# Kernel tuning notes

Measured on AMD Instinct MI355X. Metric: run time of the kernel, lower is better.

## Reference

```python
import jax, jax.numpy as jnp
import numpy as np
from jax import lax

DIM, DIN, NST, DTR, K = 96, 192, 16, 6, 4
B, H, W = 2, 56, 56
MID, SEMID = 24, 24
EPS = 1e-5


def _ln(x, g, b):
    m = x.mean(-1, keepdims=True)
    v = ((x - m) ** 2).mean(-1, keepdims=True)
    return (x - m) / jnp.sqrt(v + EPS) * g + b


def _bn(x, g, b, m, v):  # eval-mode BatchNorm2d, NCHW
    return (x - m[None, :, None, None]) / jnp.sqrt(v[None, :, None, None] + EPS) * g[None, :, None, None] + b[None, :, None, None]


def _conv(x, w, pad, groups=1):
    return lax.conv_general_dilated(x, w, (1, 1), [(pad, pad), (pad, pad)],
                                    dimension_numbers=('NCHW', 'OIHW', 'NCHW'),
                                    feature_group_count=groups)


def _vssm(xn, in_proj_w, conv_w, conv_b, x_proj_w, dt_proj_w, dt_proj_b,
          A_log, Ds, out_norm_g, out_norm_b, out_proj_w):
    Bz, Hh, Ww, C = xn.shape
    L = Hh * Ww
    xz = xn @ in_proj_w.T                      # (B,H,W,2*Din)
    xc, z = jnp.split(xz, 2, axis=-1)
    xc = xc.transpose(0, 3, 1, 2)              # (B,Din,H,W)
    xc = _conv(xc, conv_w, pad=1, groups=DIN) + conv_b[None, :, None, None]
    xc = jax.nn.silu(xc)
    # 4 scan directions: row-major, col-major, and their reverses
    x1 = xc.reshape(Bz, DIN, L)
    x2 = xc.transpose(0, 1, 3, 2).reshape(Bz, DIN, L)
    xs = jnp.stack([x1, x2], axis=1)
    xs = jnp.concatenate([xs, jnp.flip(xs, axis=-1)], axis=1)   # (B,4,Din,L)
    x_dbl = jnp.einsum('bkdl,kcd->bkcl', xs, x_proj_w)          # (B,4,dtR+2N,L)
    dts, Bs, Cs = jnp.split(x_dbl, [DTR, DTR + NST], axis=2)
    delta = jax.nn.softplus(jnp.einsum('bkrl,kdr->bkdl', dts, dt_proj_w)
                            + dt_proj_b[None, :, :, None])      # (B,4,Din,L)
    A = -jnp.exp(A_log).reshape(K, DIN, NST)
    dA = jnp.exp(jnp.einsum('bkdl,kdn->bkdln', delta, A))       # (B,4,Din,L,N)
    dBu = jnp.einsum('bkdl,bknl,bkdl->bkdln', delta, Bs, xs)

    def comb(c1, c2):
        a1, b1 = c1
        a2, b2 = c2
        return (a1 * a2, a2 * b1 + b2)

    _, hs = lax.associative_scan(comb, (dA, dBu), axis=3)       # h_t = dA_t h_{t-1} + dBu_t
    ys = jnp.einsum('bkdln,bknl->bkdl', hs, Cs) + Ds.reshape(1, K, DIN, 1) * xs
    inv = jnp.flip(ys[:, 2:4], axis=-1)

    def t_back(y):
        return y.reshape(Bz, DIN, Ww, Hh).transpose(0, 1, 3, 2).reshape(Bz, DIN, L)

    y = ys[:, 0] + t_back(ys[:, 1]) + inv[:, 0] + t_back(inv[:, 1])
    y = y.reshape(Bz, DIN, Hh, Ww).transpose(0, 2, 3, 1)        # (B,H,W,Din)
    y = _ln(y, out_norm_g, out_norm_b) * jax.nn.silu(z)
    return y @ out_proj_w.T                                      # (B,H,W,dim)


def setup_inputs() -> dict:
    key = jax.random.key(0)
    ks = jax.random.split(key, 16)
    r = lambda k, s, sc=0.05: (jax.random.normal(k, s, dtype=jnp.float32) * sc)
    d = {}
    d['x'] = jax.random.normal(ks[0], (B, DIM, H, W), dtype=jnp.float32)
    d['norm1_g'] = jnp.ones((DIM,), jnp.float32); d['norm1_b'] = jnp.zeros((DIM,), jnp.float32)
    d['in_proj_w'] = r(ks[1], (2 * DIN, DIM))
    d['conv_w'] = r(ks[2], (DIN, 1, 3, 3), 0.2); d['conv_b'] = jnp.zeros((DIN,), jnp.float32)
    d['x_proj_w'] = r(ks[3], (K, DTR + 2 * NST, DIN))
    d['dt_proj_w'] = r(ks[4], (K, DIN, DTR), 0.2)
    d['dt_proj_b'] = jnp.full((K, DIN), -2.0, jnp.float32)
    d['A_log'] = jnp.log(jnp.broadcast_to(jnp.arange(1, NST + 1, dtype=jnp.float32), (K * DIN, NST)) + 0.0)
    d['Ds'] = jnp.ones((K * DIN,), jnp.float32)
    d['out_norm_g'] = jnp.ones((DIN,), jnp.float32); d['out_norm_b'] = jnp.zeros((DIN,), jnp.float32)
    d['out_proj_w'] = r(ks[5], (DIM, DIN))
    d['scale1'] = jnp.full((DIM,), 0.1, jnp.float32)
    d['norm2_g'] = jnp.ones((DIM,), jnp.float32); d['norm2_b'] = jnp.zeros((DIM,), jnp.float32)
    d['lc_w1'] = r(ks[6], (MID, DIM, 1, 1), 0.1)
    d['lc_g1'] = jnp.ones((MID,), jnp.float32); d['lc_b1'] = jnp.zeros((MID,), jnp.float32)
    d['lc_m1'] = jnp.zeros((MID,), jnp.float32); d['lc_v1'] = jnp.ones((MID,), jnp.float32)
    d['lc_w2'] = r(ks[7], (MID, MID, 3, 3), 0.1)
    d['lc_g2'] = jnp.ones((MID,), jnp.float32); d['lc_b2'] = jnp.zeros((MID,), jnp.float32)
    d['lc_m2'] = jnp.zeros((MID,), jnp.float32); d['lc_v2'] = jnp.ones((MID,), jnp.float32)
    d['lc_w3'] = r(ks[8], (DIM, MID, 1, 1), 0.1)
    d['lc_g3'] = jnp.ones((DIM,), jnp.float32); d['lc_b3'] = jnp.zeros((DIM,), jnp.float32)
    d['lc_m3'] = jnp.zeros((DIM,), jnp.float32); d['lc_v3'] = jnp.ones((DIM,), jnp.float32)
    d['se_w1'] = r(ks[9], (SEMID, DIM), 0.1)
    d['se_w2'] = r(ks[10], (DIM, SEMID), 0.1)
    d['scale2'] = jnp.full((DIM,), 0.1, jnp.float32)
    return d


def reference(x, norm1_g, norm1_b, in_proj_w, conv_w, conv_b, x_proj_w, dt_proj_w,
              dt_proj_b, A_log, Ds, out_norm_g, out_norm_b, out_proj_w, scale1,
              norm2_g, norm2_b, lc_w1, lc_g1, lc_b1, lc_m1, lc_v1, lc_w2, lc_g2,
              lc_b2, lc_m2, lc_v2, lc_w3, lc_g3, lc_b3, lc_m3, lc_v3, se_w1,
              se_w2, scale2):
    x_hwc = x.transpose(0, 2, 3, 1)                    # (B,H,W,C)
    vl = _vssm(_ln(x_hwc, norm1_g, norm1_b), in_proj_w, conv_w, conv_b,
               x_proj_w, dt_proj_w, dt_proj_b, A_log, Ds,
               out_norm_g, out_norm_b, out_proj_w)
    vl = vl + scale1 * x_hwc                           # scaled residual
    vb = _ln(vl, norm2_g, norm2_b).transpose(0, 3, 1, 2)  # (B,C,H,W)
    h = jax.nn.relu(_bn(_conv(vb, lc_w1, pad=0), lc_g1, lc_b1, lc_m1, lc_v1))
    h = jax.nn.relu(_bn(_conv(h, lc_w2, pad=1), lc_g2, lc_b2, lc_m2, lc_v2))
    h = _bn(_conv(h, lc_w3, pad=0), lc_g3, lc_b3, lc_m3, lc_v3)
    # SE channel attention
    w = h.mean(axis=(2, 3))                            # (B,C)
    w = jax.nn.sigmoid(jax.nn.relu(w @ se_w1.T) @ se_w2.T)
    h = h * w[:, :, None, None]
    return h + scale2[None, :, None, None] * vl.transpose(0, 3, 1, 2)
```

## Files before the change

### kernel.cpp

```cpp
#include <hip/hip_runtime.h>
#include <math.h>

#define DIMC 96
#define DINC 192
#define NSTC 16
#define DTRC 6
#define KDIR 4
#define BB   2
#define HH   56
#define WWD  56
#define LL   3136
#define NPIX (BB*LL)
#define EPSF 1e-5f
#define NCH  56
#define LC   56
#define NCHAIN (BB*KDIR*DINC)
#define NCOLS 152

#define OFF_HENDT  0u
#define OFF_SUMDT  1376256u
#define OFF_XCRAW  602112u
#define OFF_ZS     1806336u
#define OFF_XCONV  3010560u
#define OFF_DTS    4214784u
#define OFF_BCB    4365312u
#define OFF_BCC    4766720u
#define OFF_XSCANT 5168128u
#define OFF_CUMD   9985024u
#define OFF_YS     14801920u
#define OFF_YT     9985024u
#define OFF_VL     11189248u
#define OFF_H1     11791360u
#define OFF_H2     11941888u
#define OFF_POOL   12092416u
#define OFF_SEW    12092608u
#define OFF_H3     0u

__device__ __forceinline__ float siluf(float x) { return x / (1.f + __expf(-x)); }
__device__ __forceinline__ float softplusf(float x) {
    return fmaxf(x, 0.f) + __logf(1.f + __expf(-fabsf(x)));
}
__device__ __forceinline__ float fexp2(float x) {
#if __has_builtin(__builtin_amdgcn_exp2f)
    return __builtin_amdgcn_exp2f(x);
#else
    return exp2f(x);
#endif
}
#define LOG2E 1.44269504088896f

__global__ __launch_bounds__(256) void gemm1_k(const float* __restrict__ x,
                                               const float* __restrict__ g,
                                               const float* __restrict__ bt,
                                               const float* __restrict__ W,
                                               float* __restrict__ xcr,
                                               float* __restrict__ zs) {
    __shared__ float xT[64 * 97];
    __shared__ float wT[96 * 100];
    __shared__ float mA[64], iA[64];
    int row0 = blockIdx.x * 64;
    int b = row0 / LL, pos0 = row0 % LL;
    int c0 = blockIdx.y * 96;
    for (int f = threadIdx.x; f < 96 * 16; f += 256) {
        int ch = f >> 4, po = (f & 15) * 4;
        float4 v = *(const float4*)&x[((size_t)b * DIMC + ch) * LL + pos0 + po];
        xT[(po + 0) * 97 + ch] = v.x; xT[(po + 1) * 97 + ch] = v.y;
        xT[(po + 2) * 97 + ch] = v.z; xT[(po + 3) * 97 + ch] = v.w;
    }
    for (int f = threadIdx.x; f < 96 * 24; f += 256) {
        int r = f / 24, kq = (f % 24) * 4;
        *(float4*)&wT[r * 100 + kq] = *(const float4*)&W[(size_t)(c0 + r) * DIMC + kq];
    }
    __syncthreads();
    if (threadIdx.x < 64) {
        float s = 0.f, q = 0.f;
        const float* xr = &xT[threadIdx.x * 97];
        for (int c = 0; c < 96; ++c) { float v = xr[c]; s += v; q = fmaf(v, v, q); }
        float m = s * (1.f / 96.f);
        mA[threadIdx.x] = m;
        iA[threadIdx.x] = rsqrtf(q * (1.f / 96.f) - m * m + EPSF);
    }
    __syncthreads();
    for (int e = threadIdx.x; e < 64 * 96; e += 256) {
        int row = e / 96, col = e - row * 96;
        float v = xT[row * 97 + col];
        xT[row * 97 + col] = (v - mA[row]) * iA[row] * g[col] + bt[col];
    }
    __syncthreads();
    int tc = threadIdx.x & 15, tr = threadIdx.x >> 4;
    float acc[4][6] = {};
    for (int k = 0; k < 96; ++k) {
        float xv[4], wv[6];
#pragma unroll
        for (int i = 0; i < 4; ++i) xv[i] = xT[(4 * tr + i) * 97 + k];
#pragma unroll
        for (int j = 0; j < 6; ++j) wv[j] = wT[(tc + 16 * j) * 100 + k];
#pragma unroll
        for (int i = 0; i < 4; ++i)
#pragma unroll
            for (int j = 0; j < 6; ++j) acc[i][j] = fmaf(xv[i], wv[j], acc[i][j]);
    }
    int pos = pos0 + 4 * tr;
    if (c0 < DINC) {
#pragma unroll
        for (int j = 0; j < 6; ++j) {
            int col = c0 + tc + 16 * j;
            float4 v = make_float4(acc[0][j], acc[1][j], acc[2][j], acc[3][j]);
            *(float4*)&xcr[((size_t)b * DINC + col) * LL + pos] = v;
        }
    } else {
#pragma unroll
        for (int i = 0; i < 4; ++i)
#pragma unroll
            for (int j = 0; j < 6; ++j) {
                int zc = c0 - DINC + tc + 16 * j;
                zs[(size_t)(row0 + 4 * tr + i) * DINC + zc] = siluf(acc[i][j]);
            }
    }
}

__global__ __launch_bounds__(448) void dwconv_k(const float* __restrict__ xcr,
                                                const float* __restrict__ cw,
                                                const float* __restrict__ cb,
                                                float* __restrict__ xconv) {
    __shared__ float P[56 * 57];
    int bd = blockIdx.x;
    int d = bd % DINC;
    size_t base = (size_t)bd * LL;
    for (int t = threadIdx.x; t < LL; t += 448)
        P[(t / 56) * 57 + (t % 56)] = xcr[base + t];
    float wk[9];
#pragma unroll
    for (int q = 0; q < 9; ++q) wk[q] = cw[d * 9 + q];
    float bias = cb[d];
    __syncthreads();
    for (int t = threadIdx.x; t < LL; t += 448) {
        int h = t / 56, w = t % 56;
        float acc = bias;
#pragma unroll
        for (int ky = 0; ky < 3; ++ky) {
            int y = h + ky - 1;
            if ((unsigned)y >= 56u) continue;
#pragma unroll
            for (int kx = 0; kx < 3; ++kx) {
                int xq = w + kx - 1;
                if ((unsigned)xq >= 56u) continue;
                acc = fmaf(wk[ky * 3 + kx], P[y * 57 + xq], acc);
            }
        }
        xconv[base + t] = siluf(acc);
    }
}

__global__ __launch_bounds__(256) void gemmx_k(const float* __restrict__ xconv,
                                               const float* __restrict__ xpw,
                                               float* __restrict__ dts,
                                               float* __restrict__ bcB,
                                               float* __restrict__ bcC,
                                               float* __restrict__ xscanT) {
    __shared__ float xT[64 * 49];
    __shared__ float wT[NCOLS * 52];
    int row0 = blockIdx.x * 64;
    int b = row0 / LL, pos0 = row0 % LL;
    int tc = threadIdx.x & 15, tr = threadIdx.x >> 4;
    float acc[4][10] = {};
    for (int kc = 0; kc < 4; ++kc) {
        if (kc) __syncthreads();
        for (int f = threadIdx.x; f < 48 * 16; f += 256) {
            int dd = f >> 4, po = (f & 15) * 4;
            float4 v = *(const float4*)&xconv[((size_t)b * DINC + kc * 48 + dd) * LL + pos0 + po];
            xT[(po + 0) * 49 + dd] = v.x; xT[(po + 1) * 49 + dd] = v.y;
            xT[(po + 2) * 49 + dd] = v.z; xT[(po + 3) * 49 + dd] = v.w;
        }
        for (int f = threadIdx.x; f < NCOLS * 12; f += 256) {
            int r = f / 12, kq = (f % 12) * 4;
            *(float4*)&wT[r * 52 + kq] = *(const float4*)&xpw[(size_t)r * DINC + kc * 48 + kq];
        }
        __syncthreads();
        for (int k = 0; k < 48; ++k) {
            float xv[4], wv[10];
#pragma unroll
            for (int i = 0; i < 4; ++i) xv[i] = xT[(4 * tr + i) * 49 + k];
#pragma unroll
            for (int j = 0; j < 10; ++j) {
                int c = tc + 16 * j;
                wv[j] = (c < NCOLS) ? wT[c * 52 + k] : 0.f;
            }
#pragma unroll
            for (int i = 0; i < 4; ++i)
#pragma unroll
                for (int j = 0; j < 10; ++j) acc[i][j] = fmaf(xv[i], wv[j], acc[i][j]);
        }
        for (int f = threadIdx.x; f < 64 * 48; f += 256) {
            int i = f / 48, dd = f - 48 * (f / 48);
            float v = xT[i * 49 + dd];
            int pos = pos0 + i;
            int hh = pos / 56, w = pos - 56 * hh;
            int lt = w * 56 + hh;
            size_t bb = (size_t)b * KDIR;
            int col = kc * 48 + dd;
            xscanT[((bb + 0) * LL + pos) * DINC + col] = v;
            xscanT[((bb + 1) * LL + lt) * DINC + col] = v;
            xscanT[((bb + 2) * LL + (LL - 1 - pos)) * DINC + col] = v;
            xscanT[((bb + 3) * LL + (LL - 1 - lt)) * DINC + col] = v;
        }
    }
#pragma unroll
    for (int i = 0; i < 4; ++i) {
        int pos = pos0 + 4 * tr + i;
        int h = pos / 56, w = pos - 56 * h;
        int lt = w * 56 + h;
#pragma unroll
        for (int j = 0; j < 10; ++j) {
            int c = tc + 16 * j;
            if (c >= NCOLS) continue;
            int k = c / 38, idx = c - 38 * k;
            int l = (k == 0) ? pos : (k == 1) ? lt : (k == 2) ? (LL - 1 - pos) : (LL - 1 - lt);
            size_t rb = (size_t)(b * KDIR + k) * LL + l;
            float v = acc[i][j];
            if (idx < DTRC)    dts[rb * DTRC + idx] = v;
            else if (idx < 22) bcB[rb * NSTC + (idx - 6)] = v;
            else               bcC[rb * NSTC + (idx - 22)] = v;
        }
    }
}

__global__ __launch_bounds__(64) void pass1_k(const float* __restrict__ dts,
                                              const float* __restrict__ bcB,
                                              const float* __restrict__ bcC,
                                              const float* __restrict__ alog,
                                              const float* __restrict__ dtw,
                                              const float* __restrict__ dtb,
                                              const float* __restrict__ xscanT,
                                              float* __restrict__ hendT,
                                              float* __restrict__ sumdT,
                                              float* __restrict__ ysT,
                                              float* __restrict__ cumdT) {
    __shared__ float sdt[LC * 7];
    __shared__ float sB[LC * 16];
    __shared__ float sC[LC * 16];
    int blk = blockIdx.x;
    int c = blk % NCH;
    int dtile = (blk / NCH) % 3;
    int bk = blk / (NCH * 3);
    int k = bk & 3;
    int l0 = c * LC;
    int t = threadIdx.x;
    int d = dtile * 64 + t;
    const float* dsrc = dts + ((size_t)bk * LL + l0) * DTRC;
    for (int f = t; f < LC * DTRC; f += 64) sdt[(f / DTRC) * 7 + (f % DTRC)] = dsrc[f];
    const float* bB = bcB + ((size_t)bk * LL + l0) * NSTC;
    const float* bC = bcC + ((size_t)bk * LL + l0) * NSTC;
    for (int f = t; f < LC * NSTC; f += 64) { sB[f] = bB[f]; sC[f] = bC[f]; }
    float wr[DTRC];
    {
        const float* wp = dtw + ((size_t)k * DINC + d) * DTRC;
#pragma unroll
        for (int r = 0; r < DTRC; ++r) wr[r] = wp[r];
    }
    float bias = dtb[k * DINC + d];
    float An2[NSTC];
    {
        const float* ap = alog + ((size_t)(k * DINC + d)) * NSTC;
#pragma unroll
        for (int n = 0; n < NSTC; ++n) An2[n] = -__expf(ap[n]) * LOG2E;
    }
    __syncthreads();
    float h[NSTC];
#pragma unroll
    for (int n = 0; n < NSTC; ++n) h[n] = 0.f;
    float cum = 0.f;
    const float* xrow = xscanT + ((size_t)bk * LL + l0) * DINC + d;
    float* yrow = ysT + ((size_t)bk * LL + l0) * DINC + d;
    float* crow = cumdT + ((size_t)bk * LL + l0) * DINC + d;
#pragma unroll 8
    for (int s = 0; s < LC; ++s) {
        float acc = bias;
#pragma unroll
        for (int r = 0; r < DTRC; ++r) acc = fmaf(wr[r], sdt[s * 7 + r], acc);
        float dv = softplusf(acc);
        float xv = xrow[(size_t)s * DINC];
        cum += dv;
        float dx = dv * xv;
        const float4* B4 = (const float4*)&sB[s * 16];
        const float4* C4 = (const float4*)&sC[s * 16];
        float y = 0.f;
#pragma unroll
        for (int nq = 0; nq < 4; ++nq) {
            float4 Bv = B4[nq], Cv = C4[nq];
            float e0 = fexp2(An2[nq * 4 + 0] * dv);
            h[nq * 4 + 0] = fmaf(e0, h[nq * 4 + 0], dx * Bv.x);
            y = fmaf(h[nq * 4 + 0], Cv.x, y);
            float e1 = fexp2(An2[nq * 4 + 1] * dv);
            h[nq * 4 + 1] = fmaf(e1, h[nq * 4 + 1], dx * Bv.y);
            y = fmaf(h[nq * 4 + 1], Cv.y, y);
            float e2 = fexp2(An2[nq * 4 + 2] * dv);
            h[nq * 4 + 2] = fmaf(e2, h[nq * 4 + 2], dx * Bv.z);
            y = fmaf(h[nq * 4 + 2], Cv.z, y);
            float e3 = fexp2(An2[nq * 4 + 3] * dv);
            h[nq * 4 + 3] = fmaf(e3, h[nq * 4 + 3], dx * Bv.w);
            y = fmaf(h[nq * 4 + 3], Cv.w, y);
        }
        yrow[(size_t)s * DINC] = y;
        crow[(size_t)s * DINC] = cum;
    }
#pragma unroll
    for (int n = 0; n < NSTC; ++n)
        hendT[((size_t)(bk * NCH + c) * NSTC + n) * DINC + d] = h[n];
    sumdT[(size_t)(bk * NCH + c) * DINC + d] = cum;
}

__global__ __launch_bounds__(256) void scan2_k(float* __restrict__ hendT,
                                               const float* __restrict__ sumdT,
                                               const float* __restrict__ alog) {
    int gid = blockIdx.x * 256 + threadIdx.x;
    int d = gid % DINC;
    int n = (gid / DINC) % NSTC;
    int bk = gid / (DINC * NSTC);
    int k = bk & 3;
    float An2 = -__expf(alog[((size_t)(k * DINC + d)) * NSTC + n]) * LOG2E;
    float h = 0.f;
#pragma unroll 4
    for (int c = 0; c < NCH; ++c) {
        size_t idx = ((size_t)(bk * NCH + c) * NSTC + n) * DINC + d;
        float he = hendT[idx];
        float sd = sumdT[(size_t)(bk * NCH + c) * DINC + d];
        hendT[idx] = h;
        h = fmaf(fexp2(An2 * sd), h, he);
    }
}

__global__ __launch_bounds__(256) void pass2_k(const float* __restrict__ bcC,
                                               const float* __restrict__ alog,
                                               const float* __restrict__ hpreT,
                                               const float* __restrict__ cumdT,
                                               float* __restrict__ ysT) {
    __shared__ float sA2[DINC * 17];
    __shared__ float sH[DINC * 17];
    __shared__ float sC[LC * NSTC];
    int blk = blockIdx.x;
    int c = blk % NCH;
    int bk = blk / NCH;
    int k = bk & 3;
    int l0 = c * LC;
    int tid = threadIdx.x;
    const float* ap = alog + (size_t)k * DINC * NSTC;
    for (int f = tid; f < DINC * NSTC; f += 256) {
        int dq = f / NSTC, n = f % NSTC;
        sA2[dq * 17 + n] = -__expf(ap[f]) * LOG2E;
    }
    for (int f = tid; f < DINC * NSTC; f += 256) {
        int n = f / DINC, dq = f % DINC;
        sH[dq * 17 + n] = hpreT[((size_t)(bk * NCH + c) * NSTC + n) * DINC + dq];
    }
    const float* bC = bcC + ((size_t)bk * LL + l0) * NSTC;
    for (int f = tid; f < LC * NSTC; f += 256) sC[f] = bC[f];
    __syncthreads();
    for (int e = tid; e < LC * DINC; e += 256) {
        int li = e / DINC, d = e - DINC * (e / DINC);
        size_t gq = ((size_t)bk * LL + l0 + li) * DINC + d;
        float cd = cumdT[gq];
        float y = ysT[gq];
        const float* A = &sA2[d * 17];
        const float* Hp = &sH[d * 17];
        const float* Cp = &sC[li * NSTC];
#pragma unroll
        for (int n = 0; n < NSTC; ++n)
            y = fmaf(Hp[n] * fexp2(A[n] * cd), Cp[n], y);
        ysT[gq] = y;
    }
}

__global__ __launch_bounds__(256) void combine_k(const float* __restrict__ ysT,
                                                 const float* __restrict__ xscanT,
                                                 const float* __restrict__ dsv,
                                                 float* __restrict__ ytT) {
    __shared__ float sD[DINC];
    int blk = blockIdx.x;
    int p0 = (blk % 196) * 16;
    int b = blk / 196;
    int tid = threadIdx.x;
    if (tid < DINC)
        sD[tid] = dsv[tid] + dsv[DINC + tid] + dsv[2 * DINC + tid] + dsv[3 * DINC + tid];
    __syncthreads();
    size_t base = (size_t)b * KDIR * LL;
    for (int e = tid; e < 16 * DINC; e += 256) {
        int pi = e / DINC, d = e - DINC * (e / DINC);
        int pos = p0 + pi;
        int hh = pos / 56, w = pos - 56 * hh;
        int lt = w * 56 + hh;
        float y = ysT[(base + pos) * DINC + d]
                + ysT[(base + LL + lt) * DINC + d]
                + ysT[(base + 2 * LL + (LL - 1 - pos)) * DINC + d]
                + ysT[(base + 3 * LL + (LL - 1 - lt)) * DINC + d];
        float xv = xscanT[(base + pos) * DINC + d];
        ytT[((size_t)b * LL + pos) * DINC + d] = fmaf(xv, sD[d], y);
    }
}

__global__ __launch_bounds__(256) void gemm2_k(const float* __restrict__ ytT,
                                               const float* __restrict__ g,
                                               const float* __restrict__ bt,
                                               const float* __restrict__ zs,
                                               const float* __restrict__ opw,
                                               const float* __restrict__ x,
                                               const float* __restrict__ sc1,
                                               float* __restrict__ vl) {
    __shared__ float xT[64 * 193];
    __shared__ float wT[96 * 52];
    __shared__ float mA[64], iA[64];
    int row0 = blockIdx.x * 64;
    int b = row0 / LL, pos0 = row0 % LL;
    for (int f = threadIdx.x; f < 64 * 48; f += 256) {
        int r = f / 48, cq = (f % 48) * 4;
        *(float4*)&xT[r * 193 + cq] = *(const float4*)&ytT[((size_t)(row0 + r)) * DINC + cq];
    }
    __syncthreads();
    if (threadIdx.x < 64) {
        float s = 0.f, q = 0.f;
        const float* xr = &xT[threadIdx.x * 193];
        for (int c = 0; c < 192; ++c) { float v = xr[c]; s += v; q = fmaf(v, v, q); }
        float m = s * (1.f / 192.f);
        mA[threadIdx.x] = m;
        iA[threadIdx.x] = rsqrtf(q * (1.f / 192.f) - m * m + EPSF);
    }
    __syncthreads();
    for (int e = threadIdx.x; e < 64 * 192; e += 256) {
        int row = e / 192, col = e - row * 192;
        float v = xT[row * 193 + col];
        float z = zs[(size_t)row0 * DINC + e];
        xT[row * 193 + col] = ((v - mA[row]) * iA[row] * g[col] + bt[col]) * z;
    }
    int tc = threadIdx.x & 15, tr = threadIdx.x >> 4;
    float acc[4][6] = {};
    for (int kc = 0; kc < 4; ++kc) {
        __syncthreads();
        for (int f = threadIdx.x; f < 96 * 12; f += 256) {
            int r = f / 12, kq = (f % 12) * 4;
            *(float4*)&wT[r * 52 + kq] = *(const float4*)&opw[(size_t)r * DINC + kc * 48 + kq];
        }
        __syncthreads();
        for (int k = 0; k < 48; ++k) {
            float xv[4], wv[6];
#pragma unroll
            for (int i = 0; i < 4; ++i) xv[i] = xT[(4 * tr + i) * 193 + kc * 48 + k];
#pragma unroll
            for (int j = 0; j < 6; ++j) wv[j] = wT[(tc + 16 * j) * 52 + k];
#pragma unroll
            for (int i = 0; i < 4; ++i)
#pragma unroll
                for (int j = 0; j < 6; ++j) acc[i][j] = fmaf(xv[i], wv[j], acc[i][j]);
        }
    }
#pragma unroll
    for (int i = 0; i < 4; ++i) {
        int pos = pos0 + 4 * tr + i;
#pragma unroll
        for (int j = 0; j < 6; ++j) {
            int col = tc + 16 * j;
            float v = fmaf(sc1[col], x[((size_t)b * DIMC + col) * LL + pos], acc[i][j]);
            vl[(size_t)(row0 + 4 * tr + i) * DIMC + col] = v;
        }
    }
}

__global__ __launch_bounds__(256) void ln2conv1_k(const float* __restrict__ vl,
                                                  const float* __restrict__ g,
                                                  const float* __restrict__ bt,
                                                  const float* __restrict__ w1,
                                                  const float* __restrict__ g1,
                                                  const float* __restrict__ b1,
                                                  const float* __restrict__ m1,
                                                  const float* __restrict__ v1,
                                                  float* __restrict__ h1) {
    __shared__ float row[4][96];
    int wv = threadIdx.x >> 6, lane = threadIdx.x & 63;
    int pix = blockIdx.x * 4 + wv;
    const float* vr = vl + (size_t)pix * DIMC;
    float a0 = vr[lane];
    float a1 = (lane < 32) ? vr[64 + lane] : 0.f;
    float s = a0 + a1, q = a0 * a0 + a1 * a1;
    for (int o = 32; o; o >>= 1) { s += __shfl_xor(s, o, 64); q += __shfl_xor(q, o, 64); }
    float m = s * (1.f / 96.f);
    float inv = rsqrtf(q * (1.f / 96.f) - m * m + EPSF);
    row[wv][lane] = (a0 - m) * inv * g[lane] + bt[lane];
    if (lane < 32) row[wv][64 + lane] = (a1 - m) * inv * g[64 + lane] + bt[64 + lane];
    __syncthreads();
    if (lane < 24) {
        const float* wr = w1 + lane * 96;
        float acc = 0.f;
#pragma unroll 8
        for (int c = 0; c < 96; ++c) acc = fmaf(row[wv][c], wr[c], acc);
        float bn = (acc - m1[lane]) * rsqrtf(v1[lane] + EPSF) * g1[lane] + b1[lane];
        int b = pix / LL, pos = pix % LL;
        h1[((size_t)b * 24 + lane) * LL + pos] = fmaxf(bn, 0.f);
    }
}

__global__ __launch_bounds__(256) void conv2_k(const float* __restrict__ h1,
                                               const float* __restrict__ w2,
                                               const float* __restrict__ g2,
                                               const float* __restrict__ b2,
                                               const float* __restrict__ m2,
                                               const float* __restrict__ v2,
                                               float* __restrict__ h2) {
    int i = blockIdx.x * 256 + threadIdx.x;
    int pos = i % LL, mo = (i / LL) % 24, b = i / (LL * 24);
    int hh = pos / WWD, ww = pos % WWD;
    float acc = 0.f;
    for (int c = 0; c < 24; ++c) {
        const float* src = h1 + ((size_t)b * 24 + c) * LL;
        const float* wk = w2 + ((size_t)(mo * 24 + c)) * 9;
#pragma unroll
        for (int ky = 0; ky < 3; ++ky) {
            int y = hh + ky - 1;
            if ((unsigned)y >= HH) continue;
#pragma unroll
            for (int kx = 0; kx < 3; ++kx) {
                int xq = ww + kx - 1;
                if ((unsigned)xq >= WWD) continue;
                acc = fmaf(wk[ky * 3 + kx], src[y * WWD + xq], acc);
            }
        }
    }
    float bn = (acc - m2[mo]) * rsqrtf(v2[mo] + EPSF) * g2[mo] + b2[mo];
    h2[i] = fmaxf(bn, 0.f);
}

__global__ __launch_bounds__(256) void conv3_k(const float* __restrict__ h2,
                                               const float* __restrict__ w3,
                                               const float* __restrict__ g3,
                                               const float* __restrict__ b3,
                                               const float* __restrict__ m3,
                                               const float* __restrict__ v3,
                                               float* __restrict__ h3) {
    int i = blockIdx.x * 256 + threadIdx.x;
    int pos = i % LL, c = (i / LL) % DIMC, b = i / (LL * DIMC);
    const float* wr = w3 + c * 24;
    float acc = 0.f;
#pragma unroll
    for (int mo = 0; mo < 24; ++mo)
        acc = fmaf(wr[mo], h2[((size_t)b * 24 + mo) * LL + pos], acc);
    h3[i] = (acc - m3[c]) * rsqrtf(v3[c] + EPSF) * g3[c] + b3[c];
}

__global__ __launch_bounds__(256) void pool_k(const float* __restrict__ h3,
                                              float* __restrict__ pooled) {
    int bc = blockIdx.x;
    const float* p = h3 + (size_t)bc * LL;
    float s = 0.f;
    for (int i = threadIdx.x; i < LL; i += 256) s += p[i];
    for (int o = 32; o; o >>= 1) s += __shfl_xor(s, o, 64);
    __shared__ float wsum[4];
    if ((threadIdx.x & 63) == 0) wsum[threadIdx.x >> 6] = s;
    __syncthreads();
    if (threadIdx.x == 0) pooled[bc] = (wsum[0] + wsum[1] + wsum[2] + wsum[3]) * (1.f / 3136.f);
}

__global__ __launch_bounds__(128) void semlp_k(const float* __restrict__ pooled,
                                               const float* __restrict__ sw1,
                                               const float* __restrict__ sw2,
                                               float* __restrict__ sew) {
    __shared__ float pl[2][96];
    __shared__ float hid[2][24];
    for (int i = threadIdx.x; i < 192; i += 128) pl[i / 96][i % 96] = pooled[i];
    __syncthreads();
    if (threadIdx.x < 48) {
        int b = threadIdx.x / 24, mo = threadIdx.x % 24;
        float acc = 0.f;
        for (int c = 0; c < 96; ++c) acc = fmaf(pl[b][c], sw1[mo * 96 + c], acc);
        hid[b][mo] = fmaxf(acc, 0.f);
    }
    __syncthreads();
    for (int i = threadIdx.x; i < 192; i += 128) {
        int b = i / 96, c = i % 96;
        float acc = 0.f;
        for (int mo = 0; mo < 24; ++mo) acc = fmaf(hid[b][mo], sw2[c * 24 + mo], acc);
        sew[i] = 1.f / (1.f + __expf(-acc));
    }
}

__global__ __launch_bounds__(256) void final_k(const float* __restrict__ h3,
                                               const float* __restrict__ sew,
                                               const float* __restrict__ vl,
                                               const float* __restrict__ sc2,
                                               float* __restrict__ out) {
    int i = blockIdx.x * 256 + threadIdx.x;
    int pos = i % LL, c = (i / LL) % DIMC, b = i / (LL * DIMC);
    out[i] = fmaf(h3[i], sew[b * DIMC + c],
                  sc2[c] * vl[((size_t)b * LL + pos) * DIMC + c]);
}

extern "C" void kernel_launch(void* const* d_in, const int* in_sizes, int n_in,
                              void* d_out, int out_size, void* d_ws, size_t ws_size,
                              hipStream_t stream) {
    const float* x    = (const float*)d_in[0];
    const float* n1g  = (const float*)d_in[1];
    const float* n1b  = (const float*)d_in[2];
    const float* ipw  = (const float*)d_in[3];
    const float* cw   = (const float*)d_in[4];
    const float* cb   = (const float*)d_in[5];
    const float* xpw  = (const float*)d_in[6];
    const float* dtw  = (const float*)d_in[7];
    const float* dtb  = (const float*)d_in[8];
    const float* alog = (const float*)d_in[9];
    const float* dsv  = (const float*)d_in[10];
    const float* ong  = (const float*)d_in[11];
    const float* onb  = (const float*)d_in[12];
    const float* opw  = (const float*)d_in[13];
    const float* sc1  = (const float*)d_in[14];
    const float* n2g  = (const float*)d_in[15];
    const float* n2b  = (const float*)d_in[16];
    const float* w1   = (const float*)d_in[17];
    const float* g1   = (const float*)d_in[18];
    const float* b1   = (const float*)d_in[19];
    const float* m1   = (const float*)d_in[20];
    const float* v1   = (const float*)d_in[21];
    const float* w2   = (const float*)d_in[22];
    const float* g2   = (const float*)d_in[23];
    const float* b2   = (const float*)d_in[24];
    const float* m2   = (const float*)d_in[25];
    const float* v2   = (const float*)d_in[26];
    const float* w3   = (const float*)d_in[27];
    const float* g3   = (const float*)d_in[28];
    const float* b3   = (const float*)d_in[29];
    const float* m3   = (const float*)d_in[30];
    const float* v3   = (const float*)d_in[31];
    const float* sw1  = (const float*)d_in[32];
    const float* sw2  = (const float*)d_in[33];
    const float* sc2  = (const float*)d_in[34];
    float* ws = (float*)d_ws;
    float* out = (float*)d_out;

    gemm1_k<<<dim3(NPIX / 64, 4), 256, 0, stream>>>(x, n1g, n1b, ipw,
                                                    ws + OFF_XCRAW, ws + OFF_ZS);
    dwconv_k<<<BB * DINC, 448, 0, stream>>>(ws + OFF_XCRAW, cw, cb, ws + OFF_XCONV);
    gemmx_k<<<NPIX / 64, 256, 0, stream>>>(ws + OFF_XCONV, xpw, ws + OFF_DTS,
                                           ws + OFF_BCB, ws + OFF_BCC, ws + OFF_XSCANT);

    pass1_k<<<BB * KDIR * 3 * NCH, 64, 0, stream>>>(
        ws + OFF_DTS, ws + OFF_BCB, ws + OFF_BCC, alog, dtw, dtb,
        ws + OFF_XSCANT, ws + OFF_HENDT, ws + OFF_SUMDT, ws + OFF_YS, ws + OFF_CUMD);
    scan2_k<<<(NCHAIN * NSTC) / 256, 256, 0, stream>>>(ws + OFF_HENDT, ws + OFF_SUMDT, alog);
    pass2_k<<<BB * KDIR * NCH, 256, 0, stream>>>(
        ws + OFF_BCC, alog, ws + OFF_HENDT, ws + OFF_CUMD, ws + OFF_YS);

    combine_k<<<BB * 196, 256, 0, stream>>>(ws + OFF_YS, ws + OFF_XSCANT, dsv, ws + OFF_YT);
    gemm2_k<<<NPIX / 64, 256, 0, stream>>>(ws + OFF_YT, ong, onb, ws + OFF_ZS, opw, x, sc1,
                                           ws + OFF_VL);
    ln2conv1_k<<<NPIX / 4, 256, 0, stream>>>(ws + OFF_VL, n2g, n2b, w1, g1, b1, m1, v1,
                                             ws + OFF_H1);
    conv2_k<<<(BB * 24 * LL) / 256, 256, 0, stream>>>(ws + OFF_H1, w2, g2, b2, m2, v2,
                                                      ws + OFF_H2);
    conv3_k<<<(BB * DIMC * LL) / 256, 256, 0, stream>>>(ws + OFF_H2, w3, g3, b3, m3, v3,
                                                        ws + OFF_H3);
    pool_k<<<BB * DIMC, 256, 0, stream>>>(ws + OFF_H3, ws + OFF_POOL);
    semlp_k<<<1, 128, 0, stream>>>(ws + OFF_POOL, sw1, sw2, ws + OFF_SEW);
    final_k<<<(BB * DIMC * LL) / 256, 256, 0, stream>>>(ws + OFF_H3, ws + OFF_SEW, ws + OFF_VL,
                                                        sc2, out);
    (void)in_sizes; (void)n_in; (void)out_size; (void)ws_size;
}
```

Measured before the change: 268.6 us.

## Fuse four-direction combine into out-projection GEMM and shorten scan chunks

Removes the separate combine kernel: the out-projection GEMM now gathers and sums the four directional scan outputs plus the D*x skip term directly into shared memory. This avoids writing and rereading the intermediate ytT buffer and drops one launch. It also changes the chunked-scan split from 56 chunks of 56 to 98 chunks of 32, which gives more parallel chunks but enlarges the carry-propagation stage, so the workspace layout is reorganised. The fused loads are scalar gathers instead of float4, which may cost bandwidth.

```diff
diff --git a/kernel.cpp b/kernel.cpp
--- a/kernel.cpp
+++ b/kernel.cpp
@@ -12,29 +12,28 @@
 #define LL   3136
 #define NPIX (BB*LL)
 #define EPSF 1e-5f
-#define NCH  56
-#define LC   56
+#define NCH  98
+#define LC   32
 #define NCHAIN (BB*KDIR*DINC)
 #define NCOLS 152
 
+#define OFF_XCRAW  0u
+#define OFF_XCONV  1204224u
+#define OFF_ZS     2408448u
+#define OFF_DTS    3612672u
+#define OFF_BCB    3763200u
+#define OFF_BCC    4164608u
+#define OFF_XSCANT 4566016u
+#define OFF_CUMD   9382912u
+#define OFF_YS     14199808u
 #define OFF_HENDT  0u
-#define OFF_SUMDT  1376256u
-#define OFF_XCRAW  602112u
-#define OFF_ZS     1806336u
-#define OFF_XCONV  3010560u
-#define OFF_DTS    4214784u
-#define OFF_BCB    4365312u
-#define OFF_BCC    4766720u
-#define OFF_XSCANT 5168128u
-#define OFF_CUMD   9985024u
-#define OFF_YS     14801920u
-#define OFF_YT     9985024u
-#define OFF_VL     11189248u
-#define OFF_H1     11791360u
-#define OFF_H2     11941888u
-#define OFF_POOL   12092416u
-#define OFF_SEW    12092608u
-#define OFF_H3     0u
+#define OFF_SUMDT  19016704u
+#define OFF_VL     9382912u
+#define OFF_H1     9985024u
+#define OFF_H2     10135552u
+#define OFF_H3     10286080u
+#define OFF_POOL   10888192u
+#define OFF_SEW    10888384u
 
 __device__ __forceinline__ float siluf(float x) { return x / (1.f + __expf(-x)); }
 __device__ __forceinline__ float softplusf(float x) {
@@ -371,34 +370,9 @@
     }
 }
 
-__global__ __launch_bounds__(256) void combine_k(const float* __restrict__ ysT,
-                                                 const float* __restrict__ xscanT,
-                                                 const float* __restrict__ dsv,
-                                                 float* __restrict__ ytT) {
-    __shared__ float sD[DINC];
-    int blk = blockIdx.x;
-    int p0 = (blk % 196) * 16;
-    int b = blk / 196;
-    int tid = threadIdx.x;
-    if (tid < DINC)
-        sD[tid] = dsv[tid] + dsv[DINC + tid] + dsv[2 * DINC + tid] + dsv[3 * DINC + tid];
-    __syncthreads();
-    size_t base = (size_t)b * KDIR * LL;
-    for (int e = tid; e < 16 * DINC; e += 256) {
-        int pi = e / DINC, d = e - DINC * (e / DINC);
-        int pos = p0 + pi;
-        int hh = pos / 56, w = pos - 56 * hh;
-        int lt = w * 56 + hh;
-        float y = ysT[(base + pos) * DINC + d]
-                + ysT[(base + LL + lt) * DINC + d]
-                + ysT[(base + 2 * LL + (LL - 1 - pos)) * DINC + d]
-                + ysT[(base + 3 * LL + (LL - 1 - lt)) * DINC + d];
-        float xv = xscanT[(base + pos) * DINC + d];
-        ytT[((size_t)b * LL + pos) * DINC + d] = fmaf(xv, sD[d], y);
-    }
-}
-
-__global__ __launch_bounds__(256) void gemm2_k(const float* __restrict__ ytT,
+__global__ __launch_bounds__(256) void gemm2_k(const float* __restrict__ ysT,
+                                               const float* __restrict__ xscanT,
+                                               const float* __restrict__ dsv,
                                                const float* __restrict__ g,
                                                const float* __restrict__ bt,
                                                const float* __restrict__ zs,
@@ -409,11 +383,25 @@
     __shared__ float xT[64 * 193];
     __shared__ float wT[96 * 52];
     __shared__ float mA[64], iA[64];
+    __shared__ float sD[DINC];
     int row0 = blockIdx.x * 64;
     int b = row0 / LL, pos0 = row0 % LL;
-    for (int f = threadIdx.x; f < 64 * 48; f += 256) {
-        int r = f / 48, cq = (f % 48) * 4;
-        *(float4*)&xT[r * 193 + cq] = *(const float4*)&ytT[((size_t)(row0 + r)) * DINC + cq];
+    if (threadIdx.x < DINC)
+        sD[threadIdx.x] = dsv[threadIdx.x] + dsv[DINC + threadIdx.x] +
+                          dsv[2 * DINC + threadIdx.x] + dsv[3 * DINC + threadIdx.x];
+    __syncthreads();
+    size_t base = (size_t)b * KDIR * LL;
+    for (int f = threadIdx.x; f < 64 * DINC; f += 256) {
+        int r = f / DINC, d = f - DINC * (f / DINC);
+        int pos = pos0 + r;
+        int hh = pos / 56, w = pos - 56 * hh;
+        int lt = w * 56 + hh;
+        float y = ysT[(base + pos) * DINC + d]
+                + ysT[(base + LL + lt) * DINC + d]
+                + ysT[(base + 2 * LL + (LL - 1 - pos)) * DINC + d]
+                + ysT[(base + 3 * LL + (LL - 1 - lt)) * DINC + d];
+        float xv = xscanT[(base + pos) * DINC + d];
+        xT[r * 193 + d] = fmaf(xv, sD[d], y);
     }
     __syncthreads();
     if (threadIdx.x < 64) {
@@ -645,9 +633,8 @@
     pass2_k<<<BB * KDIR * NCH, 256, 0, stream>>>(
         ws + OFF_BCC, alog, ws + OFF_HENDT, ws + OFF_CUMD, ws + OFF_YS);
 
-    combine_k<<<BB * 196, 256, 0, stream>>>(ws + OFF_YS, ws + OFF_XSCANT, dsv, ws + OFF_YT);
-    gemm2_k<<<NPIX / 64, 256, 0, stream>>>(ws + OFF_YT, ong, onb, ws + OFF_ZS, opw, x, sc1,
-                                           ws + OFF_VL);
+    gemm2_k<<<NPIX / 64, 256, 0, stream>>>(ws + OFF_YS, ws + OFF_XSCANT, dsv,
+                                           ong, onb, ws + OFF_ZS, opw, x, sc1, ws + OFF_VL);
     ln2conv1_k<<<NPIX / 4, 256, 0, stream>>>(ws + OFF_VL, n2g, n2b, w1, g1, b1, m1, v1,
                                              ws + OFF_H1);
     conv2_k<<<(BB * 24 * LL) / 256, 256, 0, stream>>>(ws + OFF_H1, w2, g2, b2, m2, v2,
```

Result: faster. 252.3 us (-6.1%).
